# Performance work log

Hardware: AMD Instinct MI355X
Metric: run time of the kernel (lower is better)

The kernel has to match this reference:

```python
import jax, jax.numpy as jnp
import numpy as np

N = 1024
D = 256            # model_dims
H = D // 2         # hidden_dim = 128
L = 3              # num_levels
EPS = 1e-5


def ln(x, g, b):
    mu = jnp.mean(x, axis=-1, keepdims=True)
    v = jnp.mean((x - mu) ** 2, axis=-1, keepdims=True)
    return (x - mu) / jnp.sqrt(v + EPS) * g + b


def setup_inputs() -> dict:
    key = jax.random.key(0)
    ks = jax.random.split(key, 24)
    s = 0.02
    inp = {
        'atomic_numbers': jax.random.randint(ks[0], (N,), 0, 100),
        'positions': jax.random.normal(ks[1], (N, 3), dtype=jnp.float32) * 3.0,
        'emb': jax.random.normal(ks[2], (100, H), dtype=jnp.float32) * s,
        # distance_expansion: Linear(3, H) + SiLU + LayerNorm(H)
        'de_W': jax.random.normal(ks[3], (L, H), dtype=jnp.float32) * s,
        'de_b': jnp.zeros((H,), jnp.float32),
        'de_g': jnp.ones((H,), jnp.float32),
        'de_be': jnp.zeros((H,), jnp.float32),
        'msg_W': jax.random.normal(ks[4], (L, 2 * H, H), dtype=jnp.float32) * s,
        'msg_b': jnp.zeros((L, H), jnp.float32),
        'msg_g': jnp.ones((L, H), jnp.float32),
        'msg_be': jnp.zeros((L, H), jnp.float32),
        'upd_W': jax.random.normal(ks[5], (L, 2 * H, H), dtype=jnp.float32) * s,
        'upd_b': jnp.zeros((L, H), jnp.float32),
        'upd_g': jnp.ones((L, H), jnp.float32),
        'upd_be': jnp.zeros((L, H), jnp.float32),
        # final proj: Linear(3H, D) + LayerNorm(D)
        'fp_W': jax.random.normal(ks[6], (L * H, D), dtype=jnp.float32) * s,
        'fp_b': jnp.zeros((D,), jnp.float32),
        'fp_g': jnp.ones((D,), jnp.float32),
        'fp_be': jnp.zeros((D,), jnp.float32),
    }
    return inp


def reference(atomic_numbers, positions, emb, de_W, de_b, de_g, de_be,
              msg_W, msg_b, msg_g, msg_be, upd_W, upd_b, upd_g, upd_be,
              fp_W, fp_b, fp_g, fp_be):
    x = emb[atomic_numbers]                                    # [N,H]
    diff = positions[:, None, :] - positions[None, :, :]       # [N,N,3]
    sq = jnp.sum(diff * diff, axis=-1)
    d = jnp.where(sq > 0, jnp.sqrt(jnp.where(sq > 0, sq, 1.0)), 0.0)  # safe norm
    scales = jnp.stack([jnp.exp(-d), jnp.exp(-d / 2), jnp.exp(-d / 4)], axis=-1)  # [N,N,3]
    ew = ln(jax.nn.silu(scales @ de_W + de_b), de_g, de_be)    # [N,N,H]

    level_feats = []
    for lvl in range(L):
        Wi, Wj = msg_W[lvl, :H], msg_W[lvl, H:]
        # cat([x_i, x_j]) @ W == x_i @ Wi + x_j @ Wj
        pre = x @ Wi                                           # [N,H]
        prj = x @ Wj                                           # [N,H]
        m = ln(jax.nn.silu(pre[:, None, :] + prj[None, :, :] + msg_b[lvl]),
               msg_g[lvl], msg_be[lvl])                        # [N,N,H]
        msum = jnp.einsum('ijh,ijh->ih', m, ew)                # sum over j
        u = jnp.concatenate([x, msum], axis=-1)                # [N,2H]
        x = x + ln(jax.nn.silu(u @ upd_W[lvl] + upd_b[lvl]), upd_g[lvl], upd_be[lvl])
        level_feats.append(jnp.mean(x, axis=0))

    combined = jnp.concatenate(level_feats, axis=0)            # [3H]
    return ln(combined @ fp_W + fp_b, fp_g, fp_be)             # [D]
```

## Files before the change

### kernel.cpp

```cpp
#include <hip/hip_runtime.h>
#include <math.h>

constexpr int N_ = 1024;
constexpr int H_ = 128;
constexpr int D_ = 256;
constexpr int L_ = 3;
constexpr int NT_ = N_ / 32;
constexpr float EPS_ = 1e-5f;
constexpr float LOG2E_ = 1.44269504f;
constexpr int KLUT_ = 8192;
constexpr float DMAX_ = 40.0f;
constexpr float TSCALE_ = (KLUT_ - 1) / DMAX_;
constexpr float TMAX_ = (float)(KLUT_ - 1) - 0.001f;

typedef float v2f __attribute__((ext_vector_type(2)));

__device__ __forceinline__ float fsig(float v) {
    float e = __builtin_amdgcn_exp2f(v * -LOG2E_);
    return __builtin_amdgcn_rcpf(1.0f + e);
}

template <int CTRL>
__device__ __forceinline__ float rowadd(float x) {
    int y = __builtin_amdgcn_update_dpp(0, __float_as_int(x), CTRL, 0xF, 0xF, true);
    return x + __int_as_float(y);
}
__device__ __forceinline__ float rowreduce16(float x) {
    x = rowadd<0x128>(x);
    x = rowadd<0x124>(x);
    x = rowadd<0x122>(x);
    x = rowadd<0x121>(x);
    return x;
}

#define LD8(dst, src)                                                     \
    {                                                                     \
        float4 t0_ = *(const float4*)(src);                               \
        float4 t1_ = *(const float4*)((src) + 4);                         \
        dst[0] = t0_.x; dst[1] = t0_.y; dst[2] = t0_.z; dst[3] = t0_.w;   \
        dst[4] = t1_.x; dst[5] = t1_.y; dst[6] = t1_.z; dst[7] = t1_.w;   \
    }

#define LD8V(dst, src)                                                    \
    {                                                                     \
        float4 t0_ = *(const float4*)(src);                               \
        float4 t1_ = *(const float4*)((src) + 4);                         \
        dst[0] = (v2f){t0_.x, t0_.y}; dst[1] = (v2f){t0_.z, t0_.w};       \
        dst[2] = (v2f){t1_.x, t1_.y}; dst[3] = (v2f){t1_.z, t1_.w};       \
    }

__global__ void k_lut(const float* __restrict__ deW, const float* __restrict__ deb,
                      const float* __restrict__ deg, const float* __restrict__ debe,
                      float* __restrict__ lut) {
    int e = blockIdx.x * 4 + (threadIdx.x >> 6);
    int lane = threadIdx.x & 63;
    float d = e * (DMAX_ / (KLUT_ - 1));
    float s0 = expf(-d), s1 = expf(-0.5f * d), s2 = expf(-0.25f * d);
    float v[2];
    float sum = 0.f, ssq = 0.f;
#pragma unroll
    for (int kk = 0; kk < 2; ++kk) {
        int c = lane + 64 * kk;
        float a = s0 * deW[c] + s1 * deW[H_ + c] + s2 * deW[2 * H_ + c] + deb[c];
        float sg = 1.f / (1.f + expf(-a));
        v[kk] = a * sg;
        sum += v[kk]; ssq += v[kk] * v[kk];
    }
#pragma unroll
    for (int mask = 1; mask < 64; mask <<= 1) {
        sum += __shfl_xor(sum, mask);
        ssq += __shfl_xor(ssq, mask);
    }
    float mu = sum * (1.f / H_);
    float var = ssq * (1.f / H_) - mu * mu;
    float rstd = 1.f / sqrtf(var + EPS_);
#pragma unroll
    for (int kk = 0; kk < 2; ++kk) {
        int c = lane + 64 * kk;
        lut[e * H_ + c] = (v[kk] - mu) * rstd * deg[c] + debe[c];
    }
}

__global__ void k_embed_gemm(const int* __restrict__ an, const float* __restrict__ emb,
                             const float* __restrict__ W, const float* __restrict__ b,
                             float* __restrict__ x, float* __restrict__ preb,
                             float* __restrict__ prj) {
    int i = blockIdx.x;
    int t = threadIdx.x;
    __shared__ float xr[H_];
    if (t < H_) {
        float xv = emb[an[i] * H_ + t];
        xr[t] = xv;
        x[i * H_ + t] = xv;
    }
    __syncthreads();
    int h = t & (H_ - 1);
    int off = (t >= H_) ? H_ : 0;
    float s = 0.f;
#pragma unroll 4
    for (int k = 0; k < H_; k += 4) {
        float4 xv = *(const float4*)&xr[k];
        s = fmaf(xv.x, W[(off + k) * H_ + h], s);
        s = fmaf(xv.y, W[(off + k + 1) * H_ + h], s);
        s = fmaf(xv.z, W[(off + k + 2) * H_ + h], s);
        s = fmaf(xv.w, W[(off + k + 3) * H_ + h], s);
    }
    if (t >= H_) prj[i * H_ + h] = s;
    else         preb[i * H_ + h] = s + b[h];
}

__device__ __forceinline__ void stage(const float* __restrict__ prjR, int jt, int w,
                                      int lane, float (*buf)[512]) {
    const float* g0 = prjR + (jt + 4 * w + (lane >> 5)) * H_ + (lane & 31) * 4;
    __builtin_amdgcn_global_load_lds(
        (const __attribute__((address_space(1))) void*)g0,
        (__attribute__((address_space(3))) void*)&buf[w][0], 16, 0, 0);
    const float* g1 = g0 + 2 * H_;
    __builtin_amdgcn_global_load_lds(
        (const __attribute__((address_space(1))) void*)g1,
        (__attribute__((address_space(3))) void*)&buf[w][256], 16, 0, 0);
}

__device__ __forceinline__ void cmp_step(const v2f (&EW)[4], const float* rp,
                                         const v2f (&pbv)[4],
                                         v2f (&acc1)[4], v2f (&acc2)[4]) {
    float4 pa = *(const float4*)rp;
    float4 pb4 = *(const float4*)(rp + 4);
    v2f tm[4] = {{pa.x, pa.y}, {pa.z, pa.w}, {pb4.x, pb4.y}, {pb4.z, pb4.w}};
    v2f sum2 = {0.f, 0.f}, ssq2 = {0.f, 0.f};
#pragma unroll
    for (int k = 0; k < 4; ++k) {
        v2f wv = pbv[k] + tm[k];
        v2f sg;
        sg.x = fsig(wv.x);
        sg.y = fsig(wv.y);
        v2f vv = wv * sg;
        tm[k] = vv;
        sum2 += vv;
        ssq2 += vv * vv;
    }
    float sum = rowreduce16(sum2.x + sum2.y);
    float ssq = rowreduce16(ssq2.x + ssq2.y);
    float mu = sum * (1.f / H_);
    float var = fmaf(ssq, 1.f / H_, -mu * mu);
    float rstd = __builtin_amdgcn_rsqf(var + EPS_);
    float c1 = -mu * rstd;
    v2f rstd2 = {rstd, rstd}, c12 = {c1, c1};
#pragma unroll
    for (int k = 0; k < 4; ++k) {
        v2f t = tm[k] * rstd2 + c12;
        acc1[k] += t * EW[k];
        acc2[k] += EW[k];
    }
}

#define PAIR_BODY(T, BUFRD, BUFWR, LUTRD, LUTWR)                              \
    {                                                                         \
        if ((T) + 1 < NT_) {                                                  \
            stage(prjR, ((T) + 1) * 32, w, lane, BUFWR);                      \
            int jof_ = jinfo[((T) + 1) * 32 + p];                             \
            LD8V(LUTWR, (const float*)((const char*)lut + jof_) + cb);        \
        }                                                                     \
        __builtin_amdgcn_sched_barrier(0);                                    \
        cmp_step(LUTRD, &BUFRD[w][g * 128 + q * 8], pbv, acc1, acc2);         \
    }

__global__ __launch_bounds__(512, 4) void k_pair(
    const float* __restrict__ pos, const float* __restrict__ x,
    const float* __restrict__ prebR, const float* __restrict__ prjR,
    const float* __restrict__ lut,
    const float* __restrict__ mgp, const float* __restrict__ mbep,
    const float* __restrict__ uW, const float* __restrict__ ub,
    const float* __restrict__ ug, const float* __restrict__ ube,
    const float* __restrict__ Wn, const float* __restrict__ bn,
    float* __restrict__ xout, float* __restrict__ lmean,
    float* __restrict__ prebW, float* __restrict__ prjW) {
    const int i = blockIdx.x;
    const int tid = threadIdx.x;
    const int w = tid >> 6;
    const int lane = tid & 63;
    const int g = lane >> 4;
    const int q = lane & 15;
    const int p = w * 4 + g;
    const int cb = q * 8;

    __shared__ float bufA[8][512];
    __shared__ float bufB[8][512];
    __shared__ int jinfo[N_];
    __shared__ float red[32][H_];
    __shared__ float msums[H_], xrow[H_], xs[H_];
    __shared__ float part[4][H_];
    __shared__ float r4[2][2];

    v2f pbv[4], acc1[4], acc2[4];
    LD8V(pbv, prebR + i * H_ + cb);
#pragma unroll
    for (int k = 0; k < 4; ++k) { acc1[k] = (v2f){0.f, 0.f}; acc2[k] = (v2f){0.f, 0.f}; }

    const float pix = pos[3 * i], piy = pos[3 * i + 1], piz = pos[3 * i + 2];
    for (int j = tid; j < N_; j += 512) {
        float dx = pix - pos[3 * j];
        float dy = piy - pos[3 * j + 1];
        float dz = piz - pos[3 * j + 2];
        float sq = fmaf(dx, dx, fmaf(dy, dy, dz * dz));
        float d = __builtin_amdgcn_sqrtf(sq);
        float tf = fminf(d * TSCALE_, TMAX_);
        int i0 = (int)(tf + 0.5f);
        jinfo[j] = i0 * (H_ * 4);
    }
    if (tid < H_) xrow[tid] = x[i * H_ + tid];
    __syncthreads();

    v2f lutA[4], lutB[4];
    stage(prjR, 0, w, lane, bufA);
    {
        int jof_ = jinfo[p];
        LD8V(lutA, (const float*)((const char*)lut + jof_) + cb);
    }
    for (int t = 0; t < NT_; t += 2) {
        PAIR_BODY(t, bufA, bufB, lutA, lutB);
        PAIR_BODY(t + 1, bufB, bufA, lutB, lutA);
    }

    v2f mgv[4], mbev[4], accv[4];
    LD8V(mgv, mgp + cb);
    LD8V(mbev, mbep + cb);
#pragma unroll
    for (int k = 0; k < 4; ++k)
        accv[k] = mgv[k] * acc1[k] + mbev[k] * acc2[k];
    *(float4*)&red[p][cb] = make_float4(accv[0].x, accv[0].y, accv[1].x, accv[1].y);
    *(float4*)&red[p][cb + 4] = make_float4(accv[2].x, accv[2].y, accv[3].x, accv[3].y);
    __syncthreads();
    if (tid < H_) {
        float s = 0.f;
#pragma unroll
        for (int pp = 0; pp < 32; ++pp) s += red[pp][tid];
        msums[tid] = s;
    }
    __syncthreads();

    int h = tid & (H_ - 1);
    int seg = tid >> 7;
    const float* src = (seg == 0) ? xrow : (seg == 1) ? xrow + 64
                     : (seg == 2) ? msums : msums + 64;
    const float* Wp = uW + (seg * 64) * H_ + h;
    float s2 = 0.f;
#pragma unroll 4
    for (int k = 0; k < 64; k += 4) {
        float4 uv = *(const float4*)&src[k];
        s2 = fmaf(uv.x, Wp[(k + 0) * H_], s2);
        s2 = fmaf(uv.y, Wp[(k + 1) * H_], s2);
        s2 = fmaf(uv.z, Wp[(k + 2) * H_], s2);
        s2 = fmaf(uv.w, Wp[(k + 3) * H_], s2);
    }
    part[seg][h] = s2;
    __syncthreads();
    float v = 0.f;
    if (tid < H_) {
        float sv = part[0][tid] + part[1][tid] + part[2][tid] + part[3][tid] + ub[tid];
        v = sv * fsig(sv);
    }
    float sum = v, ssq = v * v;
#pragma unroll
    for (int mask = 1; mask < 64; mask <<= 1) {
        sum += __shfl_xor(sum, mask);
        ssq += __shfl_xor(ssq, mask);
    }
    if (tid < H_ && (tid & 63) == 0) { r4[tid >> 6][0] = sum; r4[tid >> 6][1] = ssq; }
    __syncthreads();
    if (tid < H_) {
        sum = r4[0][0] + r4[1][0];
        ssq = r4[0][1] + r4[1][1];
        float mu = sum * (1.f / H_);
        float var = fmaf(ssq, 1.f / H_, -mu * mu);
        float rstd = rsqrtf(var + EPS_);
        float xn = xrow[tid] + fmaf((v - mu) * rstd, ug[tid], ube[tid]);
        xs[tid] = xn;
        xout[i * H_ + tid] = xn;
        atomicAdd(&lmean[tid], xn);
    }

    if (Wn) {
        __syncthreads();
        int which = tid >> 8;
        int kh = (tid >> 7) & 1;
        const float* Wp2 = Wn + (which * H_ + kh * 64) * H_ + h;
        const float* xsrc = xs + kh * 64;
        float s3 = 0.f;
#pragma unroll 4
        for (int k = 0; k < 64; k += 4) {
            float4 xv = *(const float4*)&xsrc[k];
            s3 = fmaf(xv.x, Wp2[(k + 0) * H_], s3);
            s3 = fmaf(xv.y, Wp2[(k + 1) * H_], s3);
            s3 = fmaf(xv.z, Wp2[(k + 2) * H_], s3);
            s3 = fmaf(xv.w, Wp2[(k + 3) * H_], s3);
        }
        part[(which << 1) | kh][h] = s3;
        __syncthreads();
        if (tid < 256) {
            int wh = tid >> 7, h3 = tid & 127;
            float val = part[wh * 2][h3] + part[wh * 2 + 1][h3];
            if (wh) prjW[i * H_ + h3] = val;
            else    prebW[i * H_ + h3] = val + bn[h3];
        }
    }
}

__global__ void k_final(const float* __restrict__ lmean, const float* __restrict__ fpW,
                        const float* __restrict__ fpb, const float* __restrict__ fpg,
                        const float* __restrict__ fpbe, float* __restrict__ out) {
    int t = threadIdx.x;
    __shared__ float comb[L_ * H_];
    comb[t] = lmean[t] * (1.f / N_);
    if (t < L_ * H_ - D_) comb[D_ + t] = lmean[D_ + t] * (1.f / N_);
    __syncthreads();
    float s = fpb[t];
#pragma unroll 8
    for (int k = 0; k < L_ * H_; ++k)
        s = fmaf(comb[k], fpW[k * D_ + t], s);
    float sum = s, ssq = s * s;
#pragma unroll
    for (int mask = 1; mask < 64; mask <<= 1) {
        sum += __shfl_xor(sum, mask);
        ssq += __shfl_xor(ssq, mask);
    }
    __shared__ float r4[4][2];
    int wv = t >> 6;
    if ((t & 63) == 0) { r4[wv][0] = sum; r4[wv][1] = ssq; }
    __syncthreads();
    sum = r4[0][0] + r4[1][0] + r4[2][0] + r4[3][0];
    ssq = r4[0][1] + r4[1][1] + r4[2][1] + r4[3][1];
    float mu = sum * (1.f / D_);
    float var = fmaf(ssq, 1.f / D_, -mu * mu);
    float rstd = rsqrtf(var + EPS_);
    out[t] = fmaf((s - mu) * rstd, fpg[t], fpbe[t]);
}

extern "C" void kernel_launch(void* const* d_in, const int* in_sizes, int n_in,
                              void* d_out, int out_size, void* d_ws, size_t ws_size,
                              hipStream_t stream) {
    const int*   an    = (const int*)d_in[0];
    const float* pos   = (const float*)d_in[1];
    const float* emb   = (const float*)d_in[2];
    const float* deW   = (const float*)d_in[3];
    const float* deb   = (const float*)d_in[4];
    const float* deg   = (const float*)d_in[5];
    const float* debe  = (const float*)d_in[6];
    const float* msgW  = (const float*)d_in[7];
    const float* msgb  = (const float*)d_in[8];
    const float* msgg  = (const float*)d_in[9];
    const float* msgbe = (const float*)d_in[10];
    const float* updW  = (const float*)d_in[11];
    const float* updb  = (const float*)d_in[12];
    const float* updg  = (const float*)d_in[13];
    const float* updbe = (const float*)d_in[14];
    const float* fpW   = (const float*)d_in[15];
    const float* fpb   = (const float*)d_in[16];
    const float* fpg   = (const float*)d_in[17];
    const float* fpbe  = (const float*)d_in[18];
    float* out = (float*)d_out;

    float* ws    = (float*)d_ws;
    float* x     = ws;
    float* prebA = x + N_ * H_;
    float* prjA  = prebA + N_ * H_;
    float* prebB = prjA + N_ * H_;
    float* prjB  = prebB + N_ * H_;
    float* lmean = prjB + N_ * H_;
    float* lut   = lmean + L_ * H_;

    hipMemsetAsync(lmean, 0, L_ * H_ * sizeof(float), stream);
    k_lut<<<KLUT_ / 4, 256, 0, stream>>>(deW, deb, deg, debe, lut);
    k_embed_gemm<<<N_, 256, 0, stream>>>(an, emb, msgW, msgb, x, prebA, prjA);
    for (int lvl = 0; lvl < L_; ++lvl) {
        const float* pR  = (lvl & 1) ? prebB : prebA;
        const float* prR = (lvl & 1) ? prjB  : prjA;
        float* pW  = (lvl & 1) ? prebA : prebB;
        float* prW = (lvl & 1) ? prjA  : prjB;
        const float* Wn = (lvl < L_ - 1) ? msgW + (lvl + 1) * 2 * H_ * H_ : nullptr;
        const float* bn = (lvl < L_ - 1) ? msgb + (lvl + 1) * H_ : nullptr;
        k_pair<<<N_, 512, 0, stream>>>(pos, x, pR, prR, lut,
                                       msgg + lvl * H_, msgbe + lvl * H_,
                                       updW + lvl * 2 * H_ * H_, updb + lvl * H_,
                                       updg + lvl * H_, updbe + lvl * H_,
                                       Wn, bn, x, lmean + lvl * H_, pW, prW);
    }
    k_final<<<1, D_, 0, stream>>>(lmean, fpW, fpb, fpg, fpbe, out);
}
```

Measured before the change: 246.9 us.

## Load prj rows directly into registers instead of staging through LDS

```diff
diff --git a/kernel.cpp b/kernel.cpp
--- a/kernel.cpp
+++ b/kernel.cpp
@@ -33,14 +33,6 @@
     return x;
 }
 
-#define LD8(dst, src)                                                     \
-    {                                                                     \
-        float4 t0_ = *(const float4*)(src);                               \
-        float4 t1_ = *(const float4*)((src) + 4);                         \
-        dst[0] = t0_.x; dst[1] = t0_.y; dst[2] = t0_.z; dst[3] = t0_.w;   \
-        dst[4] = t1_.x; dst[5] = t1_.y; dst[6] = t1_.z; dst[7] = t1_.w;   \
-    }
-
 #define LD8V(dst, src)                                                    \
     {                                                                     \
         float4 t0_ = *(const float4*)(src);                               \
@@ -109,33 +101,30 @@
     else         preb[i * H_ + h] = s + b[h];
 }
 
-__device__ __forceinline__ void stage(const float* __restrict__ prjR, int jt, int w,
-                                      int lane, float (*buf)[512]) {
-    const float* g0 = prjR + (jt + 4 * w + (lane >> 5)) * H_ + (lane & 31) * 4;
-    __builtin_amdgcn_global_load_lds(
-        (const __attribute__((address_space(1))) void*)g0,
-        (__attribute__((address_space(3))) void*)&buf[w][0], 16, 0, 0);
-    const float* g1 = g0 + 2 * H_;
-    __builtin_amdgcn_global_load_lds(
-        (const __attribute__((address_space(1))) void*)g1,
-        (__attribute__((address_space(3))) void*)&buf[w][256], 16, 0, 0);
-}
-
-__device__ __forceinline__ void cmp_step(const v2f (&EW)[4], const float* rp,
+__device__ __forceinline__ int ldjof(const int* jinfo, int t, int p, int cb4) {
+    return jinfo[(t << 5) + p] + cb4;
+}
+__device__ __forceinline__ void loadL(v2f (&dst)[4], const float* __restrict__ lut,
+                                      int jof) {
+    const float* sp = (const float*)((const char*)lut + jof);
+    LD8V(dst, sp);
+}
+__device__ __forceinline__ void loadP(v2f (&dst)[4], const float* __restrict__ prow) {
+    LD8V(dst, prow);
+}
+
+__device__ __forceinline__ void cmp_step(const v2f (&EW)[4], v2f (&TM)[4],
                                          const v2f (&pbv)[4],
                                          v2f (&acc1)[4], v2f (&acc2)[4]) {
-    float4 pa = *(const float4*)rp;
-    float4 pb4 = *(const float4*)(rp + 4);
-    v2f tm[4] = {{pa.x, pa.y}, {pa.z, pa.w}, {pb4.x, pb4.y}, {pb4.z, pb4.w}};
     v2f sum2 = {0.f, 0.f}, ssq2 = {0.f, 0.f};
 #pragma unroll
     for (int k = 0; k < 4; ++k) {
-        v2f wv = pbv[k] + tm[k];
+        v2f wv = pbv[k] + TM[k];
         v2f sg;
         sg.x = fsig(wv.x);
         sg.y = fsig(wv.y);
         v2f vv = wv * sg;
-        tm[k] = vv;
+        TM[k] = vv;
         sum2 += vv;
         ssq2 += vv * vv;
     }
@@ -148,22 +137,11 @@
     v2f rstd2 = {rstd, rstd}, c12 = {c1, c1};
 #pragma unroll
     for (int k = 0; k < 4; ++k) {
-        v2f t = tm[k] * rstd2 + c12;
+        v2f t = TM[k] * rstd2 + c12;
         acc1[k] += t * EW[k];
         acc2[k] += EW[k];
     }
 }
-
-#define PAIR_BODY(T, BUFRD, BUFWR, LUTRD, LUTWR)                              \
-    {                                                                         \
-        if ((T) + 1 < NT_) {                                                  \
-            stage(prjR, ((T) + 1) * 32, w, lane, BUFWR);                      \
-            int jof_ = jinfo[((T) + 1) * 32 + p];                             \
-            LD8V(LUTWR, (const float*)((const char*)lut + jof_) + cb);        \
-        }                                                                     \
-        __builtin_amdgcn_sched_barrier(0);                                    \
-        cmp_step(LUTRD, &BUFRD[w][g * 128 + q * 8], pbv, acc1, acc2);         \
-    }
 
 __global__ __launch_bounds__(512, 4) void k_pair(
     const float* __restrict__ pos, const float* __restrict__ x,
@@ -183,10 +161,9 @@
     const int q = lane & 15;
     const int p = w * 4 + g;
     const int cb = q * 8;
-
-    __shared__ float bufA[8][512];
-    __shared__ float bufB[8][512];
-    __shared__ int jinfo[N_];
+    const int cb4 = cb * 4;
+
+    __shared__ int jinfo[N_ + 32];
     __shared__ float red[32][H_];
     __shared__ float msums[H_], xrow[H_], xs[H_];
     __shared__ float part[4][H_];
@@ -208,19 +185,34 @@
         int i0 = (int)(tf + 0.5f);
         jinfo[j] = i0 * (H_ * 4);
     }
+    if (tid < 32) jinfo[N_ + tid] = 0;
     if (tid < H_) xrow[tid] = x[i * H_ + tid];
     __syncthreads();
 
-    v2f lutA[4], lutB[4];
-    stage(prjR, 0, w, lane, bufA);
-    {
-        int jof_ = jinfo[p];
-        LD8V(lutA, (const float*)((const char*)lut + jof_) + cb);
-    }
-    for (int t = 0; t < NT_; t += 2) {
-        PAIR_BODY(t, bufA, bufB, lutA, lutB);
-        PAIR_BODY(t + 1, bufB, bufA, lutB, lutA);
-    }
+    const float* prjRow = prjR + p * H_ + cb;
+    v2f lutA[4], lutB[4], tmA[4], tmB[4];
+    int jofA = ldjof(jinfo, 0, p, cb4);
+    int jofB = ldjof(jinfo, 1, p, cb4);
+    loadL(lutA, lut, jofA); loadP(tmA, prjRow);
+    jofA = ldjof(jinfo, 2, p, cb4);
+    __builtin_amdgcn_sched_barrier(0);
+    for (int t = 0; t < NT_ - 2; t += 2) {
+        loadL(lutB, lut, jofB); loadP(tmB, prjRow + (t + 1) * (32 * H_));
+        jofB = ldjof(jinfo, t + 3, p, cb4);
+        __builtin_amdgcn_sched_barrier(0);
+        cmp_step(lutA, tmA, pbv, acc1, acc2);
+        __builtin_amdgcn_sched_barrier(0);
+        loadL(lutA, lut, jofA); loadP(tmA, prjRow + (t + 2) * (32 * H_));
+        jofA = ldjof(jinfo, t + 4, p, cb4);
+        __builtin_amdgcn_sched_barrier(0);
+        cmp_step(lutB, tmB, pbv, acc1, acc2);
+        __builtin_amdgcn_sched_barrier(0);
+    }
+    loadL(lutB, lut, jofB); loadP(tmB, prjRow + 31 * (32 * H_));
+    __builtin_amdgcn_sched_barrier(0);
+    cmp_step(lutA, tmA, pbv, acc1, acc2);
+    __builtin_amdgcn_sched_barrier(0);
+    cmp_step(lutB, tmB, pbv, acc1, acc2);
 
     v2f mgv[4], mbev[4], accv[4];
     LD8V(mgv, mgp + cb);
```

Measured after the change: 224.1 us. -9.2%, faster.
